# Kernel tuning notes

Hardware: AMD Instinct MI355X
Metric: run time of the kernel (lower is better)

The kernel has to match this reference:

```python
import jax, jax.numpy as jnp
import numpy as np
from jax import lax

T = 1_000_000  # time steps
K = 64         # hidden states


def setup_inputs() -> dict:
    key = jax.random.key(0)
    k1, k2, k3, k4 = jax.random.split(key, 4)
    return {
        "y": jax.random.normal(k1, (T,), dtype=jnp.float32),
        "transition_logits": jax.random.normal(k2, (K, K), dtype=jnp.float32),
        "mu": jax.random.normal(k3, (K,), dtype=jnp.float32),
        "log_sigma": jax.random.normal(k4, (K,), dtype=jnp.float32) * 0.1,
    }


def _stationary_distribution(P):
    # Solve pi^T P = pi^T with sum(pi) = 1 via a linear system (differentiable).
    k = P.shape[0]
    A = jnp.transpose(P) - jnp.eye(k, dtype=P.dtype)
    A = A.at[-1, :].set(jnp.ones((k,), dtype=P.dtype))
    b = jnp.zeros((k,), dtype=P.dtype).at[-1].set(1.0)
    return jnp.linalg.solve(A, b)


def reference(y, transition_logits, mu, log_sigma):
    # Row-stochastic transition matrix [K, K]
    P = jax.nn.softmax(transition_logits, axis=-1)
    sigma = jnp.exp(log_sigma)  # [K]
    # Univariate Gaussian emission densities g[t, k] = N(y_t; mu_k, sigma_k^2)
    z = (y[:, None] - mu[None, :]) / sigma[None, :]           # [T, K]
    inv_norm = 1.0 / (sigma * jnp.sqrt(2.0 * jnp.pi))         # [K]
    g = jnp.exp(-0.5 * z * z) * inv_norm[None, :]             # [T, K]

    ut0 = _stationary_distribution(P)        # initial (predicted) distribution
    g0 = g[0]
    ft0 = jnp.sum(ut0 * g0)                  # normalizer at t=0
    utt0 = ut0 * g0 / ft0                    # filtered distribution at t=0

    def step(utt, gt):
        ut = utt @ P                         # predict: [K]
        num = ut * gt
        ft = jnp.sum(num)
        utt_new = num / ft                   # update (normalize)
        return utt_new, (ut, ft, utt_new)

    _, (Ut, ft_rest, Utt) = lax.scan(step, utt0, g[1:])

    ut = jnp.concatenate([ut0[None, :], Ut], axis=0)        # [T, K] predicted
    u_norm = jnp.concatenate([utt0[None, :], Utt], axis=0)  # [T, K] filtered
    ft = jnp.concatenate([ft0[None], ft_rest], axis=0)      # [T] normalizers
    return ut, u_norm, ft
```

## Files before the change

kernel.cpp:

```cpp
#include <hip/hip_runtime.h>

#define K 64
#define S_CHUNK 128
#define W_BURN 96
#define BATCH 16

typedef __attribute__((ext_vector_type(4))) _Float16 half4;
typedef __attribute__((ext_vector_type(4))) float f32x4;

__device__ __forceinline__ float waveReduceSum(float v) {
#pragma unroll
    for (int off = 32; off > 0; off >>= 1) v += __shfl_xor(v, off, 64);
    return v;
}

#define WS_P     0
#define WS_PI    4096
#define WS_UTT0  4160
#define WS_ISG   4224
#define WS_NNU   4288
#define WS_L2N   4352

__global__ __launch_bounds__(64) void hmm_setup(
    const float* __restrict__ y, const float* __restrict__ logits,
    const float* __restrict__ mu, const float* __restrict__ log_sigma,
    float* __restrict__ out, float* __restrict__ ws, int T)
{
    __shared__ float P[K][K];
    __shared__ float pib[K];
    const int k = threadIdx.x;

    float row[K]; float m = -3.4e38f;
#pragma unroll
    for (int i = 0; i < K; ++i) { row[i] = logits[k*K + i]; m = fmaxf(m, row[i]); }
    float s = 0.f;
#pragma unroll
    for (int i = 0; i < K; ++i) { row[i] = __expf(row[i] - m); s += row[i]; }
    float inv = 1.0f / s;
#pragma unroll
    for (int i = 0; i < K; ++i) { float p = row[i]*inv; P[k][i] = p; ws[WS_P + k*K + i] = p; }
    __syncthreads();

    pib[k] = 1.0f/64.0f;
    __syncthreads();
    for (int it = 0; it < 64; ++it) {
        float acc = 0.f;
#pragma unroll
        for (int j = 0; j < K; ++j) acc += pib[j]*P[j][k];
        float tot = waveReduceSum(acc);
        acc /= tot;
        __syncthreads();
        pib[k] = acc;
        __syncthreads();
    }
    float pi_k = pib[k];

    float mu_k = mu[k];
    float isg = __expf(-log_sigma[k]);
    float inorm = isg * 0.39894228040143267f;

    ws[WS_PI  + k] = pi_k;
    ws[WS_ISG + k] = isg;
    ws[WS_NNU + k] = -mu_k * isg;
    ws[WS_L2N + k] = __log2f(inorm);

    float y0 = y[0];
    float z = (y0 - mu_k) * isg;
    float g0 = __expf(-0.5f*z*z) * inorm;
    float num = pi_k * g0;
    float ft0 = waveReduceSum(num);
    float utt0 = num / ft0;
    ws[WS_UTT0 + k] = utt0;

    out[k] = pi_k;
    out[(size_t)T*K + k] = utt0;
    if (k == 0) out[(size_t)2*T*K] = ft0;
}

__global__ __launch_bounds__(64) void hmm_scan(
    const float* __restrict__ y, const float* __restrict__ ws,
    float* __restrict__ out, int T)
{
    const int lane = threadIdx.x;
    const int c = lane & 15;
    const int q = lane >> 4;
    const int NCH = (T + S_CHUNK - 1) / S_CHUNK;
    (void)NCH;
    const int cg = blockIdx.x * BATCH + c;
    const int t0 = cg * S_CHUNK;

    half4 a[4][4];
#pragma unroll
    for (int nb = 0; nb < 4; ++nb)
#pragma unroll
        for (int kb = 0; kb < 4; ++kb)
#pragma unroll
            for (int j = 0; j < 4; ++j)
                a[nb][kb][j] = (_Float16)ws[WS_P + (16*kb + 4*q + j)*K + 16*nb + c];

    f32x4 isg_[4], nnu_[4], l2n_[4];
#pragma unroll
    for (int nb = 0; nb < 4; ++nb)
#pragma unroll
        for (int r = 0; r < 4; ++r) {
            int s = 16*nb + 4*q + r;
            isg_[nb][r] = ws[WS_ISG + s];
            nnu_[nb][r] = ws[WS_NNU + s];
            l2n_[nb][r] = ws[WS_L2N + s];
        }

    half4 bfr[4], u0h[4];
#pragma unroll
    for (int kb = 0; kb < 4; ++kb)
#pragma unroll
        for (int j = 0; j < 4; ++j) {
            int s = 16*kb + 4*q + j;
            bfr[kb][j] = (_Float16)ws[WS_PI + s];
            u0h[kb][j] = (_Float16)ws[WS_UTT0 + s];
        }

    const int tlo = (cg == 0) ? 1 : 0;
    int tcur = t0 - W_BURN;

    float* po = out + (size_t)t0 * K + 4*q;
    float* pu = po + (size_t)T * K;
    float* pf = out + (size_t)2 * T * K + t0;

    int ib = min(max(tcur, 0), T - 4);
    f32x4 yv = *(const f32x4*)(y + ib);

#define STEP(OUTP, YCUR) do {                                                  \
    f32x4 accA_[4] = {{0.f,0.f,0.f,0.f},{0.f,0.f,0.f,0.f},                     \
                      {0.f,0.f,0.f,0.f},{0.f,0.f,0.f,0.f}};                    \
    f32x4 accB_[4] = {{0.f,0.f,0.f,0.f},{0.f,0.f,0.f,0.f},                     \
                      {0.f,0.f,0.f,0.f},{0.f,0.f,0.f,0.f}};                    \
    _Pragma("unroll")                                                          \
    for (int nb_ = 0; nb_ < 4; ++nb_)                                          \
        accA_[nb_] = __builtin_amdgcn_mfma_f32_16x16x16f16(a[nb_][0], bfr[0], accA_[nb_], 0,0,0); \
    _Pragma("unroll")                                                          \
    for (int nb_ = 0; nb_ < 4; ++nb_)                                          \
        accB_[nb_] = __builtin_amdgcn_mfma_f32_16x16x16f16(a[nb_][2], bfr[2], accB_[nb_], 0,0,0); \
    _Pragma("unroll")                                                          \
    for (int nb_ = 0; nb_ < 4; ++nb_)                                          \
        accA_[nb_] = __builtin_amdgcn_mfma_f32_16x16x16f16(a[nb_][1], bfr[1], accA_[nb_], 0,0,0); \
    _Pragma("unroll")                                                          \
    for (int nb_ = 0; nb_ < 4; ++nb_)                                          \
        accB_[nb_] = __builtin_amdgcn_mfma_f32_16x16x16f16(a[nb_][3], bfr[3], accB_[nb_], 0,0,0); \
    const bool pred = (tcur >= tlo) & (tcur < T);                              \
    f32x4 acc_[4];                                                             \
    _Pragma("unroll")                                                          \
    for (int nb_ = 0; nb_ < 4; ++nb_) acc_[nb_] = accA_[nb_] + accB_[nb_];     \
    if (OUTP && pred) {                                                        \
        _Pragma("unroll")                                                      \
        for (int nb_ = 0; nb_ < 4; ++nb_)                                      \
            *(f32x4*)(po + 16*nb_) = acc_[nb_];                                \
    }                                                                          \
    f32x4 nrm[4]; float st = 0.f;                                              \
    _Pragma("unroll")                                                          \
    for (int nb_ = 0; nb_ < 4; ++nb_) {                                        \
        _Pragma("unroll")                                                      \
        for (int r_ = 0; r_ < 4; ++r_) {                                       \
            float z  = fmaf(YCUR, isg_[nb_][r_], nnu_[nb_][r_]);               \
            float ag = fmaf(z*z, -0.72134752f, l2n_[nb_][r_]);                 \
            float g  = __builtin_amdgcn_exp2f(ag);                             \
            nrm[nb_][r_] = acc_[nb_][r_] * g;                                  \
            st += nrm[nb_][r_];                                                \
        }                                                                      \
    }                                                                          \
    st += __shfl_xor(st, 16, 64);                                              \
    st += __shfl_xor(st, 32, 64);                                              \
    const float rs = __builtin_amdgcn_rcpf(st);                                \
    _Pragma("unroll")                                                          \
    for (int nb_ = 0; nb_ < 4; ++nb_) nrm[nb_] *= rs;                          \
    if (OUTP && pred) {                                                        \
        _Pragma("unroll")                                                      \
        for (int nb_ = 0; nb_ < 4; ++nb_)                                      \
            *(f32x4*)(pu + 16*nb_) = nrm[nb_];                                 \
        if (lane < 16) *pf = st;                                               \
    }                                                                          \
    _Pragma("unroll")                                                          \
    for (int kb_ = 0; kb_ < 4; ++kb_) {                                        \
        auto lo_ = __builtin_amdgcn_cvt_pkrtz(nrm[kb_][0], nrm[kb_][1]);       \
        auto hi_ = __builtin_amdgcn_cvt_pkrtz(nrm[kb_][2], nrm[kb_][3]);       \
        bfr[kb_][0] = (_Float16)lo_[0]; bfr[kb_][1] = (_Float16)lo_[1];        \
        bfr[kb_][2] = (_Float16)hi_[0]; bfr[kb_][3] = (_Float16)hi_[1];        \
    }                                                                          \
    if (OUTP) { po += K; pu += K; pf += 1; }                                   \
    ++tcur;                                                                    \
} while (0)

#pragma unroll 1
    for (int gi = 0; gi < W_BURN/4; ++gi) {
        int ibn = min(max(tcur + 4, 0), T - 4);
        f32x4 yn = *(const f32x4*)(y + ibn);
        STEP(0, yv[0]); STEP(0, yv[1]); STEP(0, yv[2]); STEP(0, yv[3]);
        yv = yn;
    }
    {
        int ibn = min(max(tcur + 4, 0), T - 4);
        f32x4 yn = *(const f32x4*)(y + ibn);
        STEP(1, yv[0]);
        if (cg == 0) { bfr[0]=u0h[0]; bfr[1]=u0h[1]; bfr[2]=u0h[2]; bfr[3]=u0h[3]; }
        STEP(1, yv[1]); STEP(1, yv[2]); STEP(1, yv[3]);
        yv = yn;
    }
#pragma unroll 1
    for (int gi = 1; gi < S_CHUNK/4; ++gi) {
        int ibn = min(max(tcur + 4, 0), T - 4);
        f32x4 yn = *(const f32x4*)(y + ibn);
        STEP(1, yv[0]); STEP(1, yv[1]); STEP(1, yv[2]); STEP(1, yv[3]);
        yv = yn;
    }
#undef STEP
}

extern "C" void kernel_launch(void* const* d_in, const int* in_sizes, int n_in,
                              void* d_out, int out_size, void* d_ws, size_t ws_size,
                              hipStream_t stream) {
    const float* y      = (const float*)d_in[0];
    const float* logits = (const float*)d_in[1];
    const float* mu     = (const float*)d_in[2];
    const float* lsig   = (const float*)d_in[3];
    float* out = (float*)d_out;
    float* ws  = (float*)d_ws;
    const int T = in_sizes[0];

    hmm_setup<<<1, 64, 0, stream>>>(y, logits, mu, lsig, out, ws, T);

    const int nch  = (T + S_CHUNK - 1) / S_CHUNK;
    const int nblk = (nch + BATCH - 1) / BATCH;
    hmm_scan<<<nblk, 64, 0, stream>>>(y, ws, out, T);
}
```

Measured before the change: 202.1 us.

## Stage scan outputs in LDS and flush coalesced 4-step rows to global

```diff
diff --git a/kernel.cpp b/kernel.cpp
--- a/kernel.cpp
+++ b/kernel.cpp
@@ -81,13 +81,18 @@
     const float* __restrict__ y, const float* __restrict__ ws,
     float* __restrict__ out, int T)
 {
+    __shared__ float lut[16][260];
+    __shared__ float lun[16][260];
+    __shared__ float lft[16][4];
     const int lane = threadIdx.x;
     const int c = lane & 15;
     const int q = lane >> 4;
-    const int NCH = (T + S_CHUNK - 1) / S_CHUNK;
-    (void)NCH;
     const int cg = blockIdx.x * BATCH + c;
     const int t0 = cg * S_CHUNK;
+    (void)t0;
+
+    float* const ou_ = out + (size_t)T * K;
+    float* const of_ = out + (size_t)2 * T * K;
 
     half4 a[4][4];
 #pragma unroll
@@ -119,17 +124,11 @@
             u0h[kb][j] = (_Float16)ws[WS_UTT0 + s];
         }
 
-    const int tlo = (cg == 0) ? 1 : 0;
     int tcur = t0 - W_BURN;
-
-    float* po = out + (size_t)t0 * K + 4*q;
-    float* pu = po + (size_t)T * K;
-    float* pf = out + (size_t)2 * T * K + t0;
-
     int ib = min(max(tcur, 0), T - 4);
     f32x4 yv = *(const f32x4*)(y + ib);
 
-#define STEP(OUTP, YCUR) do {                                                  \
+#define STEP(OUTP, YCUR, II) do {                                              \
     f32x4 accA_[4] = {{0.f,0.f,0.f,0.f},{0.f,0.f,0.f,0.f},                     \
                       {0.f,0.f,0.f,0.f},{0.f,0.f,0.f,0.f}};                    \
     f32x4 accB_[4] = {{0.f,0.f,0.f,0.f},{0.f,0.f,0.f,0.f},                     \
@@ -146,14 +145,13 @@
     _Pragma("unroll")                                                          \
     for (int nb_ = 0; nb_ < 4; ++nb_)                                          \
         accB_[nb_] = __builtin_amdgcn_mfma_f32_16x16x16f16(a[nb_][3], bfr[3], accB_[nb_], 0,0,0); \
-    const bool pred = (tcur >= tlo) & (tcur < T);                              \
     f32x4 acc_[4];                                                             \
     _Pragma("unroll")                                                          \
     for (int nb_ = 0; nb_ < 4; ++nb_) acc_[nb_] = accA_[nb_] + accB_[nb_];     \
-    if (OUTP && pred) {                                                        \
+    if (OUTP) {                                                                \
         _Pragma("unroll")                                                      \
         for (int nb_ = 0; nb_ < 4; ++nb_)                                      \
-            *(f32x4*)(po + 16*nb_) = acc_[nb_];                                \
+            *(f32x4*)&lut[c][(II)*64 + 16*nb_ + 4*q] = acc_[nb_];              \
     }                                                                          \
     f32x4 nrm[4]; float st = 0.f;                                              \
     _Pragma("unroll")                                                          \
@@ -172,11 +170,11 @@
     const float rs = __builtin_amdgcn_rcpf(st);                                \
     _Pragma("unroll")                                                          \
     for (int nb_ = 0; nb_ < 4; ++nb_) nrm[nb_] *= rs;                          \
-    if (OUTP && pred) {                                                        \
+    if (OUTP) {                                                                \
         _Pragma("unroll")                                                      \
         for (int nb_ = 0; nb_ < 4; ++nb_)                                      \
-            *(f32x4*)(pu + 16*nb_) = nrm[nb_];                                 \
-        if (lane < 16) *pf = st;                                               \
+            *(f32x4*)&lun[c][(II)*64 + 16*nb_ + 4*q] = nrm[nb_];               \
+        if (lane < 16) lft[lane][(II)] = st;                                   \
     }                                                                          \
     _Pragma("unroll")                                                          \
     for (int kb_ = 0; kb_ < 4; ++kb_) {                                        \
@@ -185,33 +183,59 @@
         bfr[kb_][0] = (_Float16)lo_[0]; bfr[kb_][1] = (_Float16)lo_[1];        \
         bfr[kb_][2] = (_Float16)hi_[0]; bfr[kb_][3] = (_Float16)hi_[1];        \
     }                                                                          \
-    if (OUTP) { po += K; pu += K; pf += 1; }                                   \
     ++tcur;                                                                    \
+} while (0)
+
+#define FLUSH(TB) do {                                                         \
+    const int rowb_ = blockIdx.x * (BATCH * S_CHUNK) + (TB);                   \
+    const bool sp_ = (blockIdx.x == 0) && ((TB) == 0);                         \
+    _Pragma("unroll")                                                          \
+    for (int j_ = 0; j_ < 16; ++j_) {                                          \
+        int row_ = rowb_ + j_ * S_CHUNK;                                       \
+        if (row_ < T) {                                                        \
+            f32x4 vu_ = *(const f32x4*)&lut[j_][lane * 4];                     \
+            f32x4 vn_ = *(const f32x4*)&lun[j_][lane * 4];                     \
+            size_t off_ = (size_t)row_ * K + lane * 4;                         \
+            if (!(sp_ && (j_ == 0) && (lane < 16))) {                          \
+                *(f32x4*)(out + off_) = vu_;                                   \
+                *(f32x4*)(ou_ + off_) = vn_;                                   \
+            }                                                                  \
+        }                                                                      \
+    }                                                                          \
+    {                                                                          \
+        int jf_ = lane >> 2, if_ = lane & 3;                                   \
+        int rowf_ = rowb_ + jf_ * S_CHUNK;                                     \
+        float fv_ = lft[jf_][if_];                                             \
+        if ((rowf_ < T) && !(sp_ && (lane == 0))) of_[rowf_ + if_] = fv_;      \
+    }                                                                          \
 } while (0)
 
 #pragma unroll 1
     for (int gi = 0; gi < W_BURN/4; ++gi) {
         int ibn = min(max(tcur + 4, 0), T - 4);
         f32x4 yn = *(const f32x4*)(y + ibn);
-        STEP(0, yv[0]); STEP(0, yv[1]); STEP(0, yv[2]); STEP(0, yv[3]);
+        STEP(0, yv[0], 0); STEP(0, yv[1], 1); STEP(0, yv[2], 2); STEP(0, yv[3], 3);
         yv = yn;
     }
     {
         int ibn = min(max(tcur + 4, 0), T - 4);
         f32x4 yn = *(const f32x4*)(y + ibn);
-        STEP(1, yv[0]);
+        STEP(1, yv[0], 0);
         if (cg == 0) { bfr[0]=u0h[0]; bfr[1]=u0h[1]; bfr[2]=u0h[2]; bfr[3]=u0h[3]; }
-        STEP(1, yv[1]); STEP(1, yv[2]); STEP(1, yv[3]);
+        STEP(1, yv[1], 1); STEP(1, yv[2], 2); STEP(1, yv[3], 3);
+        FLUSH(0);
         yv = yn;
     }
 #pragma unroll 1
     for (int gi = 1; gi < S_CHUNK/4; ++gi) {
         int ibn = min(max(tcur + 4, 0), T - 4);
         f32x4 yn = *(const f32x4*)(y + ibn);
-        STEP(1, yv[0]); STEP(1, yv[1]); STEP(1, yv[2]); STEP(1, yv[3]);
+        STEP(1, yv[0], 0); STEP(1, yv[1], 1); STEP(1, yv[2], 2); STEP(1, yv[3], 3);
+        FLUSH(gi * 4);
         yv = yn;
     }
 #undef STEP
+#undef FLUSH
 }
 
 extern "C" void kernel_launch(void* const* d_in, const int* in_sizes, int n_in,
```

After: 206.3 us. +2.1%, slower.

## Stagger chunk start times per lane column and load y per step

Applied to the files above, without the earlier changes.

```diff
diff --git a/kernel.cpp b/kernel.cpp
--- a/kernel.cpp
+++ b/kernel.cpp
@@ -84,10 +84,11 @@
     const int lane = threadIdx.x;
     const int c = lane & 15;
     const int q = lane >> 4;
-    const int NCH = (T + S_CHUNK - 1) / S_CHUNK;
-    (void)NCH;
     const int cg = blockIdx.x * BATCH + c;
     const int t0 = cg * S_CHUNK;
+
+    float* const ou_ = out + (size_t)T * K;
+    float* const of_ = out + (size_t)2 * T * K;
 
     half4 a[4][4];
 #pragma unroll
@@ -109,27 +110,32 @@
             l2n_[nb][r] = ws[WS_L2N + s];
         }
 
-    half4 bfr[4], u0h[4];
+    half4 bfr[4], piF[4], u0h[4];
 #pragma unroll
     for (int kb = 0; kb < 4; ++kb)
 #pragma unroll
         for (int j = 0; j < 4; ++j) {
             int s = 16*kb + 4*q + j;
-            bfr[kb][j] = (_Float16)ws[WS_PI + s];
+            piF[kb][j] = (_Float16)ws[WS_PI + s];
             u0h[kb][j] = (_Float16)ws[WS_UTT0 + s];
         }
-
-    const int tlo = (cg == 0) ? 1 : 0;
-    int tcur = t0 - W_BURN;
-
-    float* po = out + (size_t)t0 * K + 4*q;
-    float* pu = po + (size_t)T * K;
-    float* pf = out + (size_t)2 * T * K + t0;
-
-    int ib = min(max(tcur, 0), T - 4);
-    f32x4 yv = *(const f32x4*)(y + ib);
-
-#define STEP(OUTP, YCUR) do {                                                  \
+    bfr[0] = piF[0]; bfr[1] = piF[1]; bfr[2] = piF[2]; bfr[3] = piF[3];
+
+    const int tlo = (cg == 0) ? 1 : t0;
+    const int t0W = t0 - W_BURN;
+    int tcur = t0W - c;
+
+    float* po = out + (long)tcur * K + 4*q;
+    float* pu = ou_ + (long)tcur * K + 4*q;
+    float* pf = of_ + tcur;
+
+#define STEP(RST) do {                                                         \
+    float yc_ = y[min(max(tcur, 0), T - 1)];                                   \
+    if (RST) {                                                                 \
+        if (tcur == t0W) {                                                     \
+            bfr[0]=piF[0]; bfr[1]=piF[1]; bfr[2]=piF[2]; bfr[3]=piF[3];        \
+        }                                                                      \
+    }                                                                          \
     f32x4 accA_[4] = {{0.f,0.f,0.f,0.f},{0.f,0.f,0.f,0.f},                     \
                       {0.f,0.f,0.f,0.f},{0.f,0.f,0.f,0.f}};                    \
     f32x4 accB_[4] = {{0.f,0.f,0.f,0.f},{0.f,0.f,0.f,0.f},                     \
@@ -150,7 +156,7 @@
     f32x4 acc_[4];                                                             \
     _Pragma("unroll")                                                          \
     for (int nb_ = 0; nb_ < 4; ++nb_) acc_[nb_] = accA_[nb_] + accB_[nb_];     \
-    if (OUTP && pred) {                                                        \
+    if (pred) {                                                                \
         _Pragma("unroll")                                                      \
         for (int nb_ = 0; nb_ < 4; ++nb_)                                      \
             *(f32x4*)(po + 16*nb_) = acc_[nb_];                                \
@@ -160,7 +166,7 @@
     for (int nb_ = 0; nb_ < 4; ++nb_) {                                        \
         _Pragma("unroll")                                                      \
         for (int r_ = 0; r_ < 4; ++r_) {                                       \
-            float z  = fmaf(YCUR, isg_[nb_][r_], nnu_[nb_][r_]);               \
+            float z  = fmaf(yc_, isg_[nb_][r_], nnu_[nb_][r_]);                \
             float ag = fmaf(z*z, -0.72134752f, l2n_[nb_][r_]);                 \
             float g  = __builtin_amdgcn_exp2f(ag);                             \
             nrm[nb_][r_] = acc_[nb_][r_] * g;                                  \
@@ -172,7 +178,7 @@
     const float rs = __builtin_amdgcn_rcpf(st);                                \
     _Pragma("unroll")                                                          \
     for (int nb_ = 0; nb_ < 4; ++nb_) nrm[nb_] *= rs;                          \
-    if (OUTP && pred) {                                                        \
+    if (pred) {                                                                \
         _Pragma("unroll")                                                      \
         for (int nb_ = 0; nb_ < 4; ++nb_)                                      \
             *(f32x4*)(pu + 16*nb_) = nrm[nb_];                                 \
@@ -185,31 +191,26 @@
         bfr[kb_][0] = (_Float16)lo_[0]; bfr[kb_][1] = (_Float16)lo_[1];        \
         bfr[kb_][2] = (_Float16)hi_[0]; bfr[kb_][3] = (_Float16)hi_[1];        \
     }                                                                          \
-    if (OUTP) { po += K; pu += K; pf += 1; }                                   \
+    po += K; pu += K; pf += 1;                                                 \
     ++tcur;                                                                    \
 } while (0)
 
 #pragma unroll 1
-    for (int gi = 0; gi < W_BURN/4; ++gi) {
-        int ibn = min(max(tcur + 4, 0), T - 4);
-        f32x4 yn = *(const f32x4*)(y + ibn);
-        STEP(0, yv[0]); STEP(0, yv[1]); STEP(0, yv[2]); STEP(0, yv[3]);
-        yv = yn;
+    for (int gi = 0; gi < 4; ++gi) {
+        STEP(1); STEP(1); STEP(1); STEP(1);
+    }
+#pragma unroll 1
+    for (int gi = 4; gi < W_BURN/4; ++gi) {
+        STEP(0); STEP(0); STEP(0); STEP(0);
     }
     {
-        int ibn = min(max(tcur + 4, 0), T - 4);
-        f32x4 yn = *(const f32x4*)(y + ibn);
-        STEP(1, yv[0]);
+        STEP(0);
         if (cg == 0) { bfr[0]=u0h[0]; bfr[1]=u0h[1]; bfr[2]=u0h[2]; bfr[3]=u0h[3]; }
-        STEP(1, yv[1]); STEP(1, yv[2]); STEP(1, yv[3]);
-        yv = yn;
+        STEP(0); STEP(0); STEP(0);
     }
 #pragma unroll 1
-    for (int gi = 1; gi < S_CHUNK/4; ++gi) {
-        int ibn = min(max(tcur + 4, 0), T - 4);
-        f32x4 yn = *(const f32x4*)(y + ibn);
-        STEP(1, yv[0]); STEP(1, yv[1]); STEP(1, yv[2]); STEP(1, yv[3]);
-        yv = yn;
+    for (int gi = W_BURN/4 + 1; gi < (W_BURN + S_CHUNK + 16)/4; ++gi) {
+        STEP(0); STEP(0); STEP(0); STEP(0);
     }
 #undef STEP
 }
```

Measured after the change: 261.2 us. 1.29x slower.
